# Performance work log

Hardware: AMD Instinct MI355X
Metric: run time of the kernel (lower is better)

## Reference

```python
import jax, jax.numpy as jnp
import numpy as np

D_MODEL = 1024
D_FF = 4096
N_EXP = 8
TOP_K = 2


def _gelu(x):
    # torch F.gelu default is exact (erf) gelu
    return jax.nn.gelu(x, approximate=False)


def setup_inputs() -> dict:
    key = jax.random.key(0)
    ks = jax.random.split(key, 12)
    s = 0.02
    return {
        "x": jax.random.normal(ks[0], (4, 2048, D_MODEL), dtype=jnp.float32),
        "shared_w1": jax.random.normal(ks[1], (D_MODEL, D_FF), dtype=jnp.float32) * s,
        "shared_b1": jnp.zeros((D_FF,), jnp.float32),
        "shared_w2": jax.random.normal(ks[2], (D_FF, D_MODEL), dtype=jnp.float32) * s,
        "shared_b2": jnp.zeros((D_MODEL,), jnp.float32),
        "router_w": jax.random.normal(ks[3], (D_MODEL, N_EXP), dtype=jnp.float32) * s,
        "router_b": jnp.zeros((N_EXP,), jnp.float32),
        "exp_w1": jax.random.normal(ks[4], (N_EXP, D_MODEL, D_FF), dtype=jnp.float32) * s,
        "exp_b1": jnp.zeros((N_EXP, D_FF), jnp.float32),
        "exp_w2": jax.random.normal(ks[5], (N_EXP, D_FF, D_MODEL), dtype=jnp.float32) * s,
        "exp_b2": jnp.zeros((N_EXP, D_MODEL), jnp.float32),
    }


def reference(x, shared_w1, shared_b1, shared_w2, shared_b2,
              router_w, router_b, exp_w1, exp_b1, exp_w2, exp_b2):
    leading = x.shape[:-1]
    d = x.shape[-1]
    xf = x.reshape(-1, d)                                   # [T, d]
    T = xf.shape[0]

    # always-on shared FFN
    h_shared = _gelu(xf @ shared_w1 + shared_b1) @ shared_w2 + shared_b2  # [T, d]

    # router: softmax -> top-k -> renormalize
    logits = xf @ router_w + router_b                       # [T, E]
    routing = jax.nn.softmax(logits, axis=-1)
    sel_w, sel_idx = jax.lax.top_k(routing, TOP_K)          # [T, K]
    sel_w = sel_w / (jnp.sum(sel_w, axis=-1, keepdims=True) + 1e-9)

    # dense combine weights: w[t,e] = sum_k sel_w[t,k] * [sel_idx[t,k]==e]
    combine = jnp.zeros((T, N_EXP), routing.dtype)
    combine = combine.at[jnp.arange(T)[:, None], sel_idx].add(sel_w)

    # specialist residual: sum_e combine[:,e] * FFN_e(x)
    residual = jnp.zeros_like(xf)
    for e in range(N_EXP):                                  # fixed small expert loop
        h = _gelu(xf @ exp_w1[e] + exp_b1[e])               # [T, d_ff]
        y = h @ exp_w2[e] + exp_b2[e]                       # [T, d]
        residual = residual + combine[:, e:e + 1] * y

    out = h_shared + residual
    return out.reshape(*leading, d)
```

## Files before the change

### kernel.cpp

```cpp
#include <hip/hip_runtime.h>
#include <hip/hip_bf16.h>


#define D_MODEL 1024
#define D_FF    4096
#define N_EXP   8
#define T_TOK   8192

typedef _Float16 half8  __attribute__((ext_vector_type(8)));
typedef _Float16 half4v __attribute__((ext_vector_type(4)));
typedef float    floatx4 __attribute__((ext_vector_type(4)));

__device__ __forceinline__ float gelu_exact(float x) {
  return 0.5f * x * (1.0f + erff(x * 0.70710678118654752f));
}

__device__ __forceinline__ void gld_lds16(const _Float16* g, _Float16* l) {
  __builtin_amdgcn_global_load_lds(
      (const __attribute__((address_space(1))) void*)g,
      (__attribute__((address_space(3))) void*)l, 16, 0, 0);
}

__global__ void convert_f32_f16(const float* __restrict__ src,
                                _Float16* __restrict__ dst, int n4) {
  int i = blockIdx.x * blockDim.x + threadIdx.x;
  if (i >= n4) return;
  float4 v = ((const float4*)src)[i];
  half4v h;
  h[0] = (_Float16)v.x; h[1] = (_Float16)v.y;
  h[2] = (_Float16)v.z; h[3] = (_Float16)v.w;
  ((half4v*)dst)[i] = h;
}

__global__ void transpose_convert(const float* __restrict__ src,
                                  _Float16* __restrict__ dst, int R, int C) {
  const size_t msz = (size_t)R * C;
  src += msz * blockIdx.z;
  dst += msz * blockIdx.z;
  __shared__ float tile[32][33];
  int c0 = blockIdx.x * 32, r0 = blockIdx.y * 32;
  int tx = threadIdx.x, ty = threadIdx.y;
#pragma unroll
  for (int i = 0; i < 4; ++i)
    tile[ty + i * 8][tx] = src[(size_t)(r0 + ty + i * 8) * C + c0 + tx];
  __syncthreads();
#pragma unroll
  for (int i = 0; i < 4; ++i)
    dst[(size_t)(c0 + ty + i * 8) * R + r0 + tx] = (_Float16)tile[tx][ty + i * 8];
}

__global__ void router_kernel(const float* __restrict__ x,
                              const float* __restrict__ rw,
                              const float* __restrict__ rb,
                              int* __restrict__ sel_idx,
                              float* __restrict__ sel_w,
                              int* __restrict__ counts) {
  int lane = threadIdx.x & 63;
  int t = blockIdx.x * 4 + (threadIdx.x >> 6);
  const float* xr = x + (size_t)t * D_MODEL;
  float acc[N_EXP];
#pragma unroll
  for (int e = 0; e < N_EXP; ++e) acc[e] = 0.f;
  for (int k = lane; k < D_MODEL; k += 64) {
    float xv = xr[k];
    const float* w = rw + (size_t)k * N_EXP;
#pragma unroll
    for (int e = 0; e < N_EXP; ++e) acc[e] += xv * w[e];
  }
#pragma unroll
  for (int off = 32; off > 0; off >>= 1) {
#pragma unroll
    for (int e = 0; e < N_EXP; ++e)
      acc[e] += __shfl_down(acc[e], off, 64);
  }
  if (lane == 0) {
    float mx = -1e30f;
#pragma unroll
    for (int e = 0; e < N_EXP; ++e) { acc[e] += rb[e]; mx = fmaxf(mx, acc[e]); }
    float p[N_EXP], s = 0.f;
#pragma unroll
    for (int e = 0; e < N_EXP; ++e) { p[e] = expf(acc[e] - mx); s += p[e]; }
    float inv = 1.f / s;
#pragma unroll
    for (int e = 0; e < N_EXP; ++e) p[e] *= inv;
    int i0 = 0; float p0 = p[0];
#pragma unroll
    for (int e = 1; e < N_EXP; ++e) if (p[e] > p0) { p0 = p[e]; i0 = e; }
    int i1 = -1; float p1 = -1.f;
#pragma unroll
    for (int e = 0; e < N_EXP; ++e)
      if (e != i0 && p[e] > p1) { p1 = p[e]; i1 = e; }
    float s2 = p0 + p1 + 1e-9f;
    sel_idx[2 * t] = i0; sel_idx[2 * t + 1] = i1;
    sel_w[2 * t] = p0 / s2; sel_w[2 * t + 1] = p1 / s2;
    atomicAdd(&counts[i0 * 32], 1);
    atomicAdd(&counts[i1 * 32], 1);
  }
}

__global__ void scan_kernel(const int* __restrict__ counts,
                            int* __restrict__ offsets,
                            int* __restrict__ cursor) {
  if (threadIdx.x == 0) {
    int s = 0;
    for (int e = 0; e < N_EXP; ++e) {
      offsets[e] = s; cursor[e * 32] = s; s += counts[e * 32];
    }
    offsets[N_EXP] = s;
  }
}

__global__ void assign_kernel(const int* __restrict__ sel_idx,
                              const float* __restrict__ sel_w,
                              int* __restrict__ cursor,
                              int* __restrict__ rows,
                              float* __restrict__ rowW) {
  int t = blockIdx.x * blockDim.x + threadIdx.x;
  if (t >= T_TOK) return;
#pragma unroll
  for (int k = 0; k < 2; ++k) {
    int e = sel_idx[2 * t + k];
    int pos = atomicAdd(&cursor[e * 32], 1);
    rows[pos] = t;
    rowW[pos] = sel_w[2 * t + k];
  }
}

template <int MODE>
__global__ __launch_bounds__(256, 3) void gemm_kernel(
    const _Float16* __restrict__ A, const _Float16* __restrict__ Bt,
    const float* __restrict__ bias, void* __restrict__ OutP,
    const int* __restrict__ rows, const float* __restrict__ rowW,
    const int* __restrict__ counts, const int* __restrict__ offsets,
    int K, int N) {
  constexpr bool EXPERT = (MODE == 1 || MODE == 3);
  const int tid = threadIdx.x;
  const int lane = tid & 63, wid = tid >> 6;
  int e = 0, M = 0, offs = 0;
  if constexpr (EXPERT) {
    e = blockIdx.z;
    M = counts[e * 32];
    offs = offsets[e];
    if ((int)blockIdx.y * 128 >= M) return;
  }
  const int m0 = blockIdx.y * 128, n0 = blockIdx.x * 128;
  const _Float16* Bte = Bt + (size_t)e * K * N;
  const float* be = bias + (size_t)e * N;

  __shared__ __align__(16) _Float16 As[128 * 32];
  __shared__ __align__(16) _Float16 Bs[128 * 32];

  const int subrow = lane >> 2, kq = lane & 3;
  const int ca0 = 2 * wid, ca1 = 2 * wid + 1;

  int la0 = m0 + ca0 * 16 + subrow;
  int la1 = m0 + ca1 * 16 + subrow;
  size_t ga0, ga1;
  if constexpr (MODE == 1) {
    int c0i = la0 < M ? la0 : M - 1;
    int c1i = la1 < M ? la1 : M - 1;
    ga0 = (size_t)rows[offs + c0i];
    ga1 = (size_t)rows[offs + c1i];
  } else if constexpr (MODE == 3) {
    ga0 = (size_t)(offs + (la0 < M ? la0 : M - 1));
    ga1 = (size_t)(offs + (la1 < M ? la1 : M - 1));
  } else {
    ga0 = (size_t)la0; ga1 = (size_t)la1;
  }
  const _Float16* aS0 = A + ga0 * K + kq * 8;
  const _Float16* aS1 = A + ga1 * K + kq * 8;
  const _Float16* bS0 = Bte + (size_t)(n0 + ca0 * 16 + subrow) * K + kq * 8;
  const _Float16* bS1 = Bte + (size_t)(n0 + ca1 * 16 + subrow) * K + kq * 8;

  _Float16* ldsA0 = As + ca0 * 512;
  _Float16* ldsA1 = As + ca1 * 512;
  _Float16* ldsB0 = Bs + ca0 * 512;
  _Float16* ldsB1 = Bs + ca1 * 512;

  floatx4 acc[4][4] = {};

  const int wm = wid >> 1, wn = wid & 1;
  const int lr = lane & 15, qd = lane >> 4;
  const _Float16* Ard = As + (wm * 64 + lr) * 32 + qd * 8;
  const _Float16* Brd = Bs + (wn * 64 + lr) * 32 + qd * 8;

  for (int kt = 0; kt < K; kt += 32) {
    __syncthreads();
    gld_lds16(aS0, ldsA0);
    gld_lds16(aS1, ldsA1);
    gld_lds16(bS0, ldsB0);
    gld_lds16(bS1, ldsB1);
    aS0 += 32; aS1 += 32; bS0 += 32; bS1 += 32;
    asm volatile("s_waitcnt vmcnt(0)" ::: "memory");
    __syncthreads();
    half8 af[4], bf[4];
#pragma unroll
    for (int mi = 0; mi < 4; ++mi)
      af[mi] = *(const half8*)(Ard + mi * 16 * 32);
#pragma unroll
    for (int ni = 0; ni < 4; ++ni)
      bf[ni] = *(const half8*)(Brd + ni * 16 * 32);
#pragma unroll
    for (int mi = 0; mi < 4; ++mi) {
#pragma unroll
      for (int ni = 0; ni < 4; ++ni)
        acc[mi][ni] = __builtin_amdgcn_mfma_f32_16x16x32_f16(
            af[mi], bf[ni], acc[mi][ni], 0, 0, 0);
    }
  }

#pragma unroll
  for (int mi = 0; mi < 4; ++mi) {
#pragma unroll
    for (int ni = 0; ni < 4; ++ni) {
      floatx4 v = acc[mi][ni];
#pragma unroll
      for (int r = 0; r < 4; ++r) {
        int lrow = m0 + wm * 64 + mi * 16 + qd * 4 + r;
        int col = n0 + wn * 64 + ni * 16 + lr;
        float val = v[r] + be[col];
        if constexpr (MODE == 0) {
          ((_Float16*)OutP)[(size_t)lrow * N + col] = (_Float16)gelu_exact(val);
        } else if constexpr (MODE == 1) {
          if (lrow < M)
            ((_Float16*)OutP)[(size_t)(offs + lrow) * N + col] =
                (_Float16)gelu_exact(val);
        } else if constexpr (MODE == 2) {
          ((float*)OutP)[(size_t)lrow * N + col] = val;
        } else {
          if (lrow < M) {
            int tkn = rows[offs + lrow];
            float w = rowW[offs + lrow];
            atomicAdd(((float*)OutP) + (size_t)tkn * N + col, w * val);
          }
        }
      }
    }
  }
}

extern "C" void kernel_launch(void* const* d_in, const int* in_sizes, int n_in,
                              void* d_out, int out_size, void* d_ws,
                              size_t ws_size, hipStream_t stream) {
  const float* x   = (const float*)d_in[0];
  const float* sw1 = (const float*)d_in[1];
  const float* sb1 = (const float*)d_in[2];
  const float* sw2 = (const float*)d_in[3];
  const float* sb2 = (const float*)d_in[4];
  const float* rw  = (const float*)d_in[5];
  const float* rb  = (const float*)d_in[6];
  const float* ew1 = (const float*)d_in[7];
  const float* eb1 = (const float*)d_in[8];
  const float* ew2 = (const float*)d_in[9];
  const float* eb2 = (const float*)d_in[10];
  float* out = (float*)d_out;

  char* ws = (char*)d_ws;
  size_t off = 0;
  auto alloc = [&](size_t bytes) {
    void* p = ws + off;
    off += (bytes + 255) & ~(size_t)255;
    return p;
  };
  _Float16* xb   = (_Float16*)alloc((size_t)T_TOK * D_MODEL * 2);
  _Float16* sw1t = (_Float16*)alloc((size_t)D_FF * D_MODEL * 2);
  _Float16* sw2t = (_Float16*)alloc((size_t)D_MODEL * D_FF * 2);
  _Float16* ew1t = (_Float16*)alloc((size_t)N_EXP * D_FF * D_MODEL * 2);
  _Float16* ew2t = (_Float16*)alloc((size_t)N_EXP * D_MODEL * D_FF * 2);
  _Float16* H    = (_Float16*)alloc((size_t)2 * T_TOK * D_FF * 2);
  int*   sel_idx = (int*)alloc((size_t)T_TOK * 2 * 4);
  float* sel_w   = (float*)alloc((size_t)T_TOK * 2 * 4);
  int*   rows    = (int*)alloc((size_t)2 * T_TOK * 4);
  float* rowW    = (float*)alloc((size_t)2 * T_TOK * 4);
  int*   counts  = (int*)alloc(N_EXP * 32 * 4);
  int*   offsets = (int*)alloc(16 * 4);
  int*   cursor  = (int*)alloc(N_EXP * 32 * 4);
  (void)ws_size; (void)in_sizes; (void)n_in; (void)out_size;

  hipMemsetAsync(counts, 0, N_EXP * 32 * 4, stream);

  convert_f32_f16<<<(T_TOK * D_MODEL / 4 + 255) / 256, 256, 0, stream>>>(
      x, xb, T_TOK * D_MODEL / 4);
  dim3 tb(32, 8);
  transpose_convert<<<dim3(D_FF / 32, D_MODEL / 32, 1), tb, 0, stream>>>(
      sw1, sw1t, D_MODEL, D_FF);
  transpose_convert<<<dim3(D_MODEL / 32, D_FF / 32, 1), tb, 0, stream>>>(
      sw2, sw2t, D_FF, D_MODEL);
  transpose_convert<<<dim3(D_FF / 32, D_MODEL / 32, N_EXP), tb, 0, stream>>>(
      ew1, ew1t, D_MODEL, D_FF);
  transpose_convert<<<dim3(D_MODEL / 32, D_FF / 32, N_EXP), tb, 0, stream>>>(
      ew2, ew2t, D_FF, D_MODEL);

  router_kernel<<<T_TOK / 4, 256, 0, stream>>>(x, rw, rb, sel_idx, sel_w, counts);
  scan_kernel<<<1, 64, 0, stream>>>(counts, offsets, cursor);
  assign_kernel<<<T_TOK / 256, 256, 0, stream>>>(sel_idx, sel_w, cursor, rows, rowW);

  gemm_kernel<0><<<dim3(D_FF / 128, T_TOK / 128), 256, 0, stream>>>(
      xb, sw1t, sb1, H, nullptr, nullptr, nullptr, nullptr, D_MODEL, D_FF);
  gemm_kernel<2><<<dim3(D_MODEL / 128, T_TOK / 128), 256, 0, stream>>>(
      H, sw2t, sb2, out, nullptr, nullptr, nullptr, nullptr, D_FF, D_MODEL);
  gemm_kernel<1><<<dim3(D_FF / 128, T_TOK / 128, N_EXP), 256, 0, stream>>>(
      xb, ew1t, eb1, H, rows, nullptr, counts, offsets, D_MODEL, D_FF);
  gemm_kernel<3><<<dim3(D_MODEL / 128, T_TOK / 128, N_EXP), 256, 0, stream>>>(
      H, ew2t, eb2, out, rows, rowW, counts, offsets, D_FF, D_MODEL);
}
```

Measured before the change: 1.259 ms.

## Merge shared and expert GEMMs into single launches, swizzle LDS, replace atomics with combine

Shared and expert FFN GEMMs now run in one grouped launch per layer, with z=0 as the shared path and z>0 as the experts. This fills the GPU better and removes the serial gaps between launches. The K tile grows to 64 with an XOR-swizzled LDS layout to avoid bank conflicts, and launch bounds rise to 4 waves. Expert outputs go to a dense buffer (aliased onto the dead w1t region) and a separate combine kernel does the weighted sum, replacing float atomicAdd scatter. The cost is extra memory traffic for Yexp and the combine pass, plus a larger H buffer.

```diff
diff --git a/kernel.cpp b/kernel.cpp
--- a/kernel.cpp
+++ b/kernel.cpp
@@ -6,6 +6,7 @@
 #define D_FF    4096
 #define N_EXP   8
 #define T_TOK   8192
+#define BK      64
 
 typedef _Float16 half8  __attribute__((ext_vector_type(8)));
 typedef _Float16 half4v __attribute__((ext_vector_type(4)));
@@ -32,11 +33,12 @@
   ((half4v*)dst)[i] = h;
 }
 
-__global__ void transpose_convert(const float* __restrict__ src,
-                                  _Float16* __restrict__ dst, int R, int C) {
+__global__ void transpose_convert9(const float* __restrict__ srcSh,
+                                   const float* __restrict__ srcEx,
+                                   _Float16* __restrict__ dst, int R, int C) {
   const size_t msz = (size_t)R * C;
-  src += msz * blockIdx.z;
-  dst += msz * blockIdx.z;
+  const float* src = (blockIdx.z == 0) ? srcSh : srcEx + msz * (blockIdx.z - 1);
+  _Float16* d = dst + msz * blockIdx.z;
   __shared__ float tile[32][33];
   int c0 = blockIdx.x * 32, r0 = blockIdx.y * 32;
   int tx = threadIdx.x, ty = threadIdx.y;
@@ -46,7 +48,7 @@
   __syncthreads();
 #pragma unroll
   for (int i = 0; i < 4; ++i)
-    dst[(size_t)(c0 + ty + i * 8) * R + r0 + tx] = (_Float16)tile[tx][ty + i * 8];
+    d[(size_t)(c0 + ty + i * 8) * R + r0 + tx] = (_Float16)tile[tx][ty + i * 8];
 }
 
 __global__ void router_kernel(const float* __restrict__ x,
@@ -111,10 +113,9 @@
 }
 
 __global__ void assign_kernel(const int* __restrict__ sel_idx,
-                              const float* __restrict__ sel_w,
                               int* __restrict__ cursor,
                               int* __restrict__ rows,
-                              float* __restrict__ rowW) {
+                              int* __restrict__ inv) {
   int t = blockIdx.x * blockDim.x + threadIdx.x;
   if (t >= T_TOK) return;
 #pragma unroll
@@ -122,121 +123,137 @@
     int e = sel_idx[2 * t + k];
     int pos = atomicAdd(&cursor[e * 32], 1);
     rows[pos] = t;
-    rowW[pos] = sel_w[2 * t + k];
-  }
-}
-
-template <int MODE>
-__global__ __launch_bounds__(256, 3) void gemm_kernel(
-    const _Float16* __restrict__ A, const _Float16* __restrict__ Bt,
-    const float* __restrict__ bias, void* __restrict__ OutP,
-    const int* __restrict__ rows, const float* __restrict__ rowW,
-    const int* __restrict__ counts, const int* __restrict__ offsets,
-    int K, int N) {
-  constexpr bool EXPERT = (MODE == 1 || MODE == 3);
-  const int tid = threadIdx.x;
-  const int lane = tid & 63, wid = tid >> 6;
-  int e = 0, M = 0, offs = 0;
-  if constexpr (EXPERT) {
-    e = blockIdx.z;
-    M = counts[e * 32];
-    offs = offsets[e];
+    inv[2 * t + k] = pos;
+  }
+}
+
+template <int PHASE>
+__global__ __launch_bounds__(256, 4) void gemm_kernel(
+    const _Float16* __restrict__ A, const _Float16* __restrict__ Wt,
+    const float* __restrict__ biasSh, const float* __restrict__ biasEx,
+    _Float16* __restrict__ Hout, float* __restrict__ out,
+    float* __restrict__ Yexp, const int* __restrict__ rows,
+    const int* __restrict__ counts, const int* __restrict__ offsets) {
+  constexpr int K = (PHASE == 1) ? D_MODEL : D_FF;
+  constexpr int N = (PHASE == 1) ? D_FF : D_MODEL;
+  const int z = blockIdx.z;
+  int M = T_TOK, offs = 0;
+  if (z > 0) {
+    M = counts[(z - 1) * 32];
+    offs = offsets[z - 1];
     if ((int)blockIdx.y * 128 >= M) return;
   }
+  const int tid = threadIdx.x, lane = tid & 63, wid = tid >> 6;
   const int m0 = blockIdx.y * 128, n0 = blockIdx.x * 128;
-  const _Float16* Bte = Bt + (size_t)e * K * N;
-  const float* be = bias + (size_t)e * N;
-
-  __shared__ __align__(16) _Float16 As[128 * 32];
-  __shared__ __align__(16) _Float16 Bs[128 * 32];
-
-  const int subrow = lane >> 2, kq = lane & 3;
-  const int ca0 = 2 * wid, ca1 = 2 * wid + 1;
-
-  int la0 = m0 + ca0 * 16 + subrow;
-  int la1 = m0 + ca1 * 16 + subrow;
-  size_t ga0, ga1;
-  if constexpr (MODE == 1) {
-    int c0i = la0 < M ? la0 : M - 1;
-    int c1i = la1 < M ? la1 : M - 1;
-    ga0 = (size_t)rows[offs + c0i];
-    ga1 = (size_t)rows[offs + c1i];
-  } else if constexpr (MODE == 3) {
-    ga0 = (size_t)(offs + (la0 < M ? la0 : M - 1));
-    ga1 = (size_t)(offs + (la1 < M ? la1 : M - 1));
-  } else {
-    ga0 = (size_t)la0; ga1 = (size_t)la1;
-  }
-  const _Float16* aS0 = A + ga0 * K + kq * 8;
-  const _Float16* aS1 = A + ga1 * K + kq * 8;
-  const _Float16* bS0 = Bte + (size_t)(n0 + ca0 * 16 + subrow) * K + kq * 8;
-  const _Float16* bS1 = Bte + (size_t)(n0 + ca1 * 16 + subrow) * K + kq * 8;
-
-  _Float16* ldsA0 = As + ca0 * 512;
-  _Float16* ldsA1 = As + ca1 * 512;
-  _Float16* ldsB0 = Bs + ca0 * 512;
-  _Float16* ldsB1 = Bs + ca1 * 512;
+  const _Float16* Wz = Wt + (size_t)z * N * K;
+
+  __shared__ __align__(16) _Float16 As[128 * BK];
+  __shared__ __align__(16) _Float16 Bs[128 * BK];
+
+  const int sub = lane >> 3, p = lane & 7, g = p ^ sub;
+  const _Float16* aS[4];
+  const _Float16* bS[4];
+  _Float16 *ldsA[4], *ldsB[4];
+#pragma unroll
+  for (int j = 0; j < 4; ++j) {
+    const int c = wid * 4 + j;
+    const int rA = m0 + c * 8 + sub;
+    size_t gRow;
+    if constexpr (PHASE == 1) {
+      gRow = (z == 0) ? (size_t)rA
+                      : (size_t)rows[offs + (rA < M ? rA : M - 1)];
+    } else {
+      gRow = (z == 0) ? (size_t)rA
+                      : (size_t)(T_TOK + offs + (rA < M ? rA : M - 1));
+    }
+    aS[j] = A + gRow * K + g * 8;
+    bS[j] = Wz + (size_t)(n0 + c * 8 + sub) * K + g * 8;
+    ldsA[j] = As + c * 512;
+    ldsB[j] = Bs + c * 512;
+  }
 
   floatx4 acc[4][4] = {};
-
   const int wm = wid >> 1, wn = wid & 1;
   const int lr = lane & 15, qd = lane >> 4;
-  const _Float16* Ard = As + (wm * 64 + lr) * 32 + qd * 8;
-  const _Float16* Brd = Bs + (wn * 64 + lr) * 32 + qd * 8;
-
-  for (int kt = 0; kt < K; kt += 32) {
+
+  for (int kt = 0; kt < K; kt += BK) {
     __syncthreads();
-    gld_lds16(aS0, ldsA0);
-    gld_lds16(aS1, ldsA1);
-    gld_lds16(bS0, ldsB0);
-    gld_lds16(bS1, ldsB1);
-    aS0 += 32; aS1 += 32; bS0 += 32; bS1 += 32;
+#pragma unroll
+    for (int j = 0; j < 4; ++j) { gld_lds16(aS[j], ldsA[j]); gld_lds16(bS[j], ldsB[j]); }
+#pragma unroll
+    for (int j = 0; j < 4; ++j) { aS[j] += BK; bS[j] += BK; }
     asm volatile("s_waitcnt vmcnt(0)" ::: "memory");
     __syncthreads();
-    half8 af[4], bf[4];
-#pragma unroll
-    for (int mi = 0; mi < 4; ++mi)
-      af[mi] = *(const half8*)(Ard + mi * 16 * 32);
-#pragma unroll
-    for (int ni = 0; ni < 4; ++ni)
-      bf[ni] = *(const half8*)(Brd + ni * 16 * 32);
-#pragma unroll
-    for (int mi = 0; mi < 4; ++mi) {
-#pragma unroll
-      for (int ni = 0; ni < 4; ++ni)
-        acc[mi][ni] = __builtin_amdgcn_mfma_f32_16x16x32_f16(
-            af[mi], bf[ni], acc[mi][ni], 0, 0, 0);
+#pragma unroll
+    for (int h = 0; h < 2; ++h) {
+      half8 af[4], bf[4];
+#pragma unroll
+      for (int mi = 0; mi < 4; ++mi) {
+        const int r = wm * 64 + mi * 16 + lr;
+        const int slot = (h * 4 + qd) ^ (r & 7);
+        af[mi] = *(const half8*)(As + r * BK + slot * 8);
+      }
+#pragma unroll
+      for (int ni = 0; ni < 4; ++ni) {
+        const int r = wn * 64 + ni * 16 + lr;
+        const int slot = (h * 4 + qd) ^ (r & 7);
+        bf[ni] = *(const half8*)(Bs + r * BK + slot * 8);
+      }
+#pragma unroll
+      for (int mi = 0; mi < 4; ++mi)
+#pragma unroll
+        for (int ni = 0; ni < 4; ++ni)
+          acc[mi][ni] = __builtin_amdgcn_mfma_f32_16x16x32_f16(
+              af[mi], bf[ni], acc[mi][ni], 0, 0, 0);
     }
   }
 
+  const float* be = (z == 0) ? biasSh : biasEx + (size_t)(z - 1) * N;
 #pragma unroll
   for (int mi = 0; mi < 4; ++mi) {
 #pragma unroll
     for (int ni = 0; ni < 4; ++ni) {
       floatx4 v = acc[mi][ni];
 #pragma unroll
-      for (int r = 0; r < 4; ++r) {
-        int lrow = m0 + wm * 64 + mi * 16 + qd * 4 + r;
-        int col = n0 + wn * 64 + ni * 16 + lr;
-        float val = v[r] + be[col];
-        if constexpr (MODE == 0) {
-          ((_Float16*)OutP)[(size_t)lrow * N + col] = (_Float16)gelu_exact(val);
-        } else if constexpr (MODE == 1) {
-          if (lrow < M)
-            ((_Float16*)OutP)[(size_t)(offs + lrow) * N + col] =
+      for (int r4 = 0; r4 < 4; ++r4) {
+        const int lrow = m0 + wm * 64 + mi * 16 + qd * 4 + r4;
+        const int col = n0 + wn * 64 + ni * 16 + lr;
+        const float val = v[r4] + be[col];
+        if constexpr (PHASE == 1) {
+          if (z == 0) {
+            Hout[(size_t)lrow * N + col] = (_Float16)gelu_exact(val);
+          } else if (lrow < M) {
+            Hout[(size_t)(T_TOK + offs + lrow) * N + col] =
                 (_Float16)gelu_exact(val);
-        } else if constexpr (MODE == 2) {
-          ((float*)OutP)[(size_t)lrow * N + col] = val;
+          }
         } else {
-          if (lrow < M) {
-            int tkn = rows[offs + lrow];
-            float w = rowW[offs + lrow];
-            atomicAdd(((float*)OutP) + (size_t)tkn * N + col, w * val);
+          if (z == 0) {
+            out[(size_t)lrow * N + col] = val;
+          } else if (lrow < M) {
+            Yexp[(size_t)(offs + lrow) * N + col] = val;
           }
         }
       }
     }
   }
+}
+
+__global__ void combine_kernel(float* __restrict__ out,
+                               const float* __restrict__ Yexp,
+                               const int* __restrict__ inv,
+                               const float* __restrict__ selw) {
+  const int t = blockIdx.x;
+  const int c = threadIdx.x * 4;
+  const int p0 = inv[2 * t], p1 = inv[2 * t + 1];
+  const float w0 = selw[2 * t], w1 = selw[2 * t + 1];
+  float4 o = *(float4*)(out + (size_t)t * D_MODEL + c);
+  const float4 a = *(const float4*)(Yexp + (size_t)p0 * D_MODEL + c);
+  const float4 b = *(const float4*)(Yexp + (size_t)p1 * D_MODEL + c);
+  o.x += w0 * a.x + w1 * b.x;
+  o.y += w0 * a.y + w1 * b.y;
+  o.z += w0 * a.z + w1 * b.z;
+  o.w += w0 * a.w + w1 * b.w;
+  *(float4*)(out + (size_t)t * D_MODEL + c) = o;
 }
 
 extern "C" void kernel_launch(void* const* d_in, const int* in_sizes, int n_in,
@@ -262,16 +279,15 @@
     off += (bytes + 255) & ~(size_t)255;
     return p;
   };
-  _Float16* xb   = (_Float16*)alloc((size_t)T_TOK * D_MODEL * 2);
-  _Float16* sw1t = (_Float16*)alloc((size_t)D_FF * D_MODEL * 2);
-  _Float16* sw2t = (_Float16*)alloc((size_t)D_MODEL * D_FF * 2);
-  _Float16* ew1t = (_Float16*)alloc((size_t)N_EXP * D_FF * D_MODEL * 2);
-  _Float16* ew2t = (_Float16*)alloc((size_t)N_EXP * D_MODEL * D_FF * 2);
-  _Float16* H    = (_Float16*)alloc((size_t)2 * T_TOK * D_FF * 2);
+  _Float16* xb  = (_Float16*)alloc((size_t)T_TOK * D_MODEL * 2);
+  _Float16* w2t = (_Float16*)alloc((size_t)9 * D_MODEL * D_FF * 2);
+  _Float16* H   = (_Float16*)alloc((size_t)3 * T_TOK * D_FF * 2);
+  _Float16* w1t = (_Float16*)alloc((size_t)9 * D_FF * D_MODEL * 2);
+  float* Yexp   = (float*)w1t;
   int*   sel_idx = (int*)alloc((size_t)T_TOK * 2 * 4);
   float* sel_w   = (float*)alloc((size_t)T_TOK * 2 * 4);
   int*   rows    = (int*)alloc((size_t)2 * T_TOK * 4);
-  float* rowW    = (float*)alloc((size_t)2 * T_TOK * 4);
+  int*   inv     = (int*)alloc((size_t)2 * T_TOK * 4);
   int*   counts  = (int*)alloc(N_EXP * 32 * 4);
   int*   offsets = (int*)alloc(16 * 4);
   int*   cursor  = (int*)alloc(N_EXP * 32 * 4);
@@ -282,25 +298,19 @@
   convert_f32_f16<<<(T_TOK * D_MODEL / 4 + 255) / 256, 256, 0, stream>>>(
       x, xb, T_TOK * D_MODEL / 4);
   dim3 tb(32, 8);
-  transpose_convert<<<dim3(D_FF / 32, D_MODEL / 32, 1), tb, 0, stream>>>(
-      sw1, sw1t, D_MODEL, D_FF);
-  transpose_convert<<<dim3(D_MODEL / 32, D_FF / 32, 1), tb, 0, stream>>>(
-      sw2, sw2t, D_FF, D_MODEL);
-  transpose_convert<<<dim3(D_FF / 32, D_MODEL / 32, N_EXP), tb, 0, stream>>>(
-      ew1, ew1t, D_MODEL, D_FF);
-  transpose_convert<<<dim3(D_MODEL / 32, D_FF / 32, N_EXP), tb, 0, stream>>>(
-      ew2, ew2t, D_FF, D_MODEL);
+  transpose_convert9<<<dim3(D_FF / 32, D_MODEL / 32, 9), tb, 0, stream>>>(
+      sw1, ew1, w1t, D_MODEL, D_FF);
+  transpose_convert9<<<dim3(D_MODEL / 32, D_FF / 32, 9), tb, 0, stream>>>(
+      sw2, ew2, w2t, D_FF, D_MODEL);
 
   router_kernel<<<T_TOK / 4, 256, 0, stream>>>(x, rw, rb, sel_idx, sel_w, counts);
   scan_kernel<<<1, 64, 0, stream>>>(counts, offsets, cursor);
-  assign_kernel<<<T_TOK / 256, 256, 0, stream>>>(sel_idx, sel_w, cursor, rows, rowW);
-
-  gemm_kernel<0><<<dim3(D_FF / 128, T_TOK / 128), 256, 0, stream>>>(
-      xb, sw1t, sb1, H, nullptr, nullptr, nullptr, nullptr, D_MODEL, D_FF);
-  gemm_kernel<2><<<dim3(D_MODEL / 128, T_TOK / 128), 256, 0, stream>>>(
-      H, sw2t, sb2, out, nullptr, nullptr, nullptr, nullptr, D_FF, D_MODEL);
-  gemm_kernel<1><<<dim3(D_FF / 128, T_TOK / 128, N_EXP), 256, 0, stream>>>(
-      xb, ew1t, eb1, H, rows, nullptr, counts, offsets, D_MODEL, D_FF);
-  gemm_kernel<3><<<dim3(D_MODEL / 128, T_TOK / 128, N_EXP), 256, 0, stream>>>(
-      H, ew2t, eb2, out, rows, rowW, counts, offsets, D_FF, D_MODEL);
-}
+  assign_kernel<<<T_TOK / 256, 256, 0, stream>>>(sel_idx, cursor, rows, inv);
+
+  gemm_kernel<1><<<dim3(D_FF / 128, T_TOK / 128, 9), 256, 0, stream>>>(
+      xb, w1t, sb1, eb1, H, nullptr, nullptr, rows, counts, offsets);
+  gemm_kernel<2><<<dim3(D_MODEL / 128, T_TOK / 128, 9), 256, 0, stream>>>(
+      H, w2t, sb2, eb2, nullptr, out, Yexp, rows, counts, offsets);
+
+  combine_kernel<<<T_TOK, 256, 0, stream>>>(out, Yexp, inv, sel_w);
+}
```

Measured after the change: 1.658 ms. +31.7%, slower.
